# Kernel optimization log

Measured on AMD Instinct MI355X. Metric: run time of the kernel, lower is better.

Reference implementation:

```python
import jax, jax.numpy as jnp
import numpy as np

N_NODES = 50000
N_EDGES = 400000
NODE_DIM = 128
EDGE_DIM = 64
HIDDEN = 128  # must equal NODE_DIM (index_add into zeros_like(node_feat))
EPS = 1e-8


def _param(key, shape):
    fan_in = shape[0]
    return (jax.random.normal(key, shape, jnp.float32) / np.sqrt(fan_in)).astype(jnp.float32)


def setup_inputs() -> dict:
    key = jax.random.key(0)
    ks = jax.random.split(key, 20)
    inp = {
        'node_feat': jax.random.normal(ks[0], (N_NODES, NODE_DIM), jnp.float32),
        'edge_attr': jax.random.normal(ks[1], (N_EDGES, EDGE_DIM), jnp.float32),
        'coords': 5.0 * jax.random.normal(ks[2], (N_NODES, 3), jnp.float32),
        'edge_index': jax.random.randint(ks[3], (2, N_EDGES), 0, N_NODES, dtype=jnp.int32),
        # edge_mlp: Linear(2*node+edge -> hidden), SiLU, Linear(hidden -> hidden), SiLU
        'We1': _param(ks[4], (2 * NODE_DIM + EDGE_DIM, HIDDEN)),
        'be1': jnp.zeros((HIDDEN,), jnp.float32),
        'We2': _param(ks[5], (HIDDEN, HIDDEN)),
        'be2': jnp.zeros((HIDDEN,), jnp.float32),
        # node_mlp: Linear(node+hidden -> hidden), SiLU, Linear(hidden -> node)
        'Wn1': _param(ks[6], (NODE_DIM + HIDDEN, HIDDEN)),
        'bn1': jnp.zeros((HIDDEN,), jnp.float32),
        'Wn2': _param(ks[7], (HIDDEN, NODE_DIM)),
        'bn2': jnp.zeros((NODE_DIM,), jnp.float32),
        # coord_mlp: Linear(hidden -> hidden//2), SiLU, Linear(hidden//2 -> 1)
        'Wc1': _param(ks[8], (HIDDEN, HIDDEN // 2)),
        'bc1': jnp.zeros((HIDDEN // 2,), jnp.float32),
        'Wc2': _param(ks[9], (HIDDEN // 2, 1)),
        'bc2': jnp.zeros((1,), jnp.float32),
    }
    return inp


def reference(node_feat, edge_attr, coords, edge_index,
              We1, be1, We2, be2,
              Wn1, bn1, Wn2, bn2,
              Wc1, bc1, Wc2, bc2):
    src, dst = edge_index[0], edge_index[1]
    n_nodes = node_feat.shape[0]

    # gather -> edge MLP
    edge_feat = jnp.concatenate([node_feat[src], node_feat[dst], edge_attr], axis=-1)  # [E, 2*ND+ED]
    edge_message = jax.nn.silu(jax.nn.silu(edge_feat @ We1 + be1) @ We2 + be2)         # [E, H]

    # scatter-add messages to destination nodes
    aggr = jax.ops.segment_sum(edge_message, dst, num_segments=n_nodes)                # [N, H]

    # node update (residual)
    node_in = jnp.concatenate([node_feat, aggr], axis=-1)
    node_update = jax.nn.silu(node_in @ Wn1 + bn1) @ Wn2 + bn2
    updated_nodes = node_feat + node_update

    # equivariant coordinate update
    coord_w = jax.nn.silu(edge_message @ Wc1 + bc1) @ Wc2 + bc2                        # [E, 1]
    coord_diff = coords[src] - coords[dst]                                             # [E, 3]
    coord_diff = coord_diff / (jnp.linalg.norm(coord_diff, axis=-1, keepdims=True) + EPS)
    coord_update = jax.ops.segment_sum(coord_w * coord_diff, dst, num_segments=n_nodes)
    updated_coords = coords + coord_update

    return (updated_nodes, updated_coords)
```

## Files before the change

### kernel.cpp

```cpp
#include <hip/hip_runtime.h>
#include <hip/hip_bf16.h>
#include <math.h>
#include <stdint.h>

#define NN 50000
#define NE 400000

typedef __attribute__((ext_vector_type(8))) short short8;
typedef __attribute__((ext_vector_type(4))) float f32x4;

#define OFF_W1S  0
#define OFF_W1D  16384
#define OFF_W1E  32768
#define OFF_WE2T 40960
#define OFF_WN1T 57344
#define OFF_WN2T 90112
#define OFF_WC1T 106496
#define W_TOTAL  114688

__device__ __forceinline__ float silu_f(float x) {
    return x * (1.0f / (1.0f + __expf(-x)));
}
__device__ __forceinline__ short f2bf(float f) {
    __hip_bfloat16 b = __float2bfloat16(f);
    return *reinterpret_cast<short*>(&b);
}
__device__ __forceinline__ float bf2f(short s) {
    uint32_t u = ((uint32_t)(uint16_t)s) << 16;
    float f; __builtin_memcpy(&f, &u, 4); return f;
}
__device__ __forceinline__ uint32_t pk2(float lo, float hi) {
    return (uint32_t)(uint16_t)f2bf(lo) | ((uint32_t)(uint16_t)f2bf(hi) << 16);
}
__device__ __forceinline__ short8 cvt8(float4 a, float4 b) {
    short8 r;
    r[0] = f2bf(a.x); r[1] = f2bf(a.y); r[2] = f2bf(a.z); r[3] = f2bf(a.w);
    r[4] = f2bf(b.x); r[5] = f2bf(b.y); r[6] = f2bf(b.z); r[7] = f2bf(b.w);
    return r;
}

__device__ __forceinline__ short8 exch8(uint32_t e0, uint32_t e1,
                                        uint32_t o0, uint32_t o1,
                                        int g, int le) {
    const int srcA = le + 16 * ((g & 1) * 2);
    const int srcB = srcA + 16;
    const uint32_t a0e = __shfl((int)e0, srcA), a0o = __shfl((int)o0, srcA);
    const uint32_t a1e = __shfl((int)e1, srcA), a1o = __shfl((int)o1, srcA);
    const uint32_t b0e = __shfl((int)e0, srcB), b0o = __shfl((int)o0, srcB);
    const uint32_t b1e = __shfl((int)e1, srcB), b1o = __shfl((int)o1, srcB);
    const bool hi = (g & 2) != 0;
    uint32_t v[4];
    v[0] = hi ? a0o : a0e;  v[1] = hi ? a1o : a1e;
    v[2] = hi ? b0o : b0e;  v[3] = hi ? b1o : b1e;
    short8 r; __builtin_memcpy(&r, v, 16); return r;
}

__global__ void zero_kernel(float4* __restrict__ p, int n4) {
    int i = blockIdx.x * blockDim.x + threadIdx.x;
    int st = gridDim.x * blockDim.x;
    for (; i < n4; i += st) p[i] = make_float4(0.f, 0.f, 0.f, 0.f);
}

__global__ __launch_bounds__(256) void prep_kernel(
    const float* __restrict__ We1, const float* __restrict__ We2,
    const float* __restrict__ Wn1, const float* __restrict__ Wn2,
    const float* __restrict__ Wc1, short* __restrict__ wb)
{
    const int i = blockIdx.x * 256 + threadIdx.x;
    if (i >= W_TOTAL) return;
    float v; int rel, n, k;
    if (i < OFF_W1D)       { rel = i;            n = rel >> 7; k = rel & 127; v = We1[k * 128 + n]; }
    else if (i < OFF_W1E)  { rel = i - OFF_W1D;  n = rel >> 7; k = rel & 127; v = We1[(k + 128) * 128 + n]; }
    else if (i < OFF_WE2T) { rel = i - OFF_W1E;  n = rel >> 6; k = rel & 63;  v = We1[(k + 256) * 128 + n]; }
    else if (i < OFF_WN1T) { rel = i - OFF_WE2T; n = rel >> 7; k = rel & 127; v = We2[k * 128 + n]; }
    else if (i < OFF_WN2T) { rel = i - OFF_WN1T; n = rel >> 8; k = rel & 255; v = Wn1[k * 128 + n]; }
    else if (i < OFF_WC1T) { rel = i - OFF_WN2T; n = rel >> 7; k = rel & 127; v = Wn2[k * 128 + n]; }
    else                   { rel = i - OFF_WC1T; n = rel >> 7; k = rel & 127; v = Wc1[k * 64 + n]; }
    wb[i] = f2bf(v);
}

__global__ __launch_bounds__(256, 4) void ynode_kernel(
    const float* __restrict__ nf, const short* __restrict__ wb,
    short* __restrict__ ysb, short* __restrict__ ydb)
{
    const int tid = threadIdx.x;
    const int wv = tid >> 6, lane = tid & 63, le = lane & 15, grp = lane >> 4;
    const int nb = blockIdx.x * 128, wbase = wv * 32;
    const int row0 = min(nb + wbase + le, NN - 1);
    const int row1 = min(nb + wbase + 16 + le, NN - 1);

    #pragma unroll 1
    for (int pass = 0; pass < 2; ++pass) {
        const short* wt = wb + (pass ? OFF_W1D : OFF_W1S);
        short* op = pass ? ydb : ysb;

        f32x4 acc[2][8];
        #pragma unroll
        for (int m = 0; m < 2; ++m)
            #pragma unroll
            for (int t = 0; t < 8; ++t) acc[m][t] = (f32x4){0.f, 0.f, 0.f, 0.f};

        #pragma unroll
        for (int kc = 0; kc < 4; ++kc) {
            const int gk = kc * 32 + grp * 8;
            const float* p0 = nf + (size_t)row0 * 128 + gk;
            const float* p1 = nf + (size_t)row1 * 128 + gk;
            const short8 a0 = cvt8(*(const float4*)p0, *(const float4*)(p0 + 4));
            const short8 a1 = cvt8(*(const float4*)p1, *(const float4*)(p1 + 4));
            short8 bfv[8];
            #pragma unroll
            for (int t = 0; t < 8; ++t)
                bfv[t] = *(const short8*)(wt + (size_t)(t * 16 + le) * 128 + gk);
            #pragma unroll
            for (int t = 0; t < 8; ++t) {
                acc[0][t] = __builtin_amdgcn_mfma_f32_16x16x32_bf16(a0, bfv[t], acc[0][t], 0, 0, 0);
                acc[1][t] = __builtin_amdgcn_mfma_f32_16x16x32_bf16(a1, bfv[t], acc[1][t], 0, 0, 0);
            }
        }
        #pragma unroll
        for (int t = 0; t < 8; ++t)
            #pragma unroll
            for (int m = 0; m < 2; ++m)
                #pragma unroll
                for (int r = 0; r < 4; ++r) {
                    const int row = nb + wbase + m * 16 + grp * 4 + r;
                    if (row < NN)
                        op[(size_t)row * 128 + t * 16 + le] = f2bf(acc[m][t][r]);
                }
    }
}

__global__ __launch_bounds__(256, 4) void edge_kernel(
    const short* __restrict__ ysb, const short* __restrict__ ydb,
    const float* __restrict__ ea, const float* __restrict__ coords,
    const int* __restrict__ ei, const short* __restrict__ wb,
    const float* __restrict__ be1, const float* __restrict__ be2,
    const float* __restrict__ bc1, const float* __restrict__ bc2,
    const float* __restrict__ Wc2f,
    float* __restrict__ aggr, float* __restrict__ coord_acc)
{
    __shared__ float Ht4[4][16 * 136];

    const int tid = threadIdx.x;
    const int wv = tid >> 6, lane = tid & 63, le = lane & 15, g = lane >> 4;
    const int e = (blockIdx.x * 4 + wv) * 16 + le;
    float* Ht = Ht4[wv];

    const int s0 = ei[e], d0 = ei[NE + e];

    short8 ys8[4], yd8[4];
    #pragma unroll
    for (int cc = 0; cc < 4; ++cc) {
        ys8[cc] = *(const short8*)(ysb + (size_t)s0 * 128 + cc * 32 + g * 8);
        yd8[cc] = *(const short8*)(ydb + (size_t)d0 * 128 + cc * 32 + g * 8);
    }

    short8 eaB[2];
    #pragma unroll
    for (int kc = 0; kc < 2; ++kc) {
        const float* pe = ea + (size_t)e * 64 + kc * 32 + g * 8;
        eaB[kc] = cvt8(*(const float4*)pe, *(const float4*)(pe + 4));
    }

    f32x4 acc[8];
    #pragma unroll
    for (int t = 0; t < 8; ++t) acc[t] = (f32x4){0.f, 0.f, 0.f, 0.f};

    const short* w1e = wb + OFF_W1E;
    #pragma unroll
    for (int kc = 0; kc < 2; ++kc) {
        const int gk = kc * 32 + g * 8;
        short8 wfv[8];
        #pragma unroll
        for (int t = 0; t < 8; ++t)
            wfv[t] = *(const short8*)(w1e + (size_t)(t * 16 + le) * 64 + gk);
        #pragma unroll
        for (int t = 0; t < 8; ++t)
            acc[t] = __builtin_amdgcn_mfma_f32_16x16x32_bf16(wfv[t], eaB[kc], acc[t], 0, 0, 0);
    }

    uint32_t hp[8][2];
    #pragma unroll
    for (int t = 0; t < 8; ++t) {
        hp[t][0] = pk2(acc[t][0], acc[t][1]);
        hp[t][1] = pk2(acc[t][2], acc[t][3]);
    }

    short8 h1f[4];
    #pragma unroll
    for (int cc = 0; cc < 4; ++cc) {
        const short8 ex = exch8(hp[cc*2][0], hp[cc*2][1], hp[cc*2+1][0], hp[cc*2+1][1], g, le);
        const float* bp = be1 + cc * 32 + g * 8;
        #pragma unroll
        for (int j = 0; j < 8; ++j)
            h1f[cc][j] = f2bf(silu_f(bf2f(ex[j]) + bf2f(ys8[cc][j]) + bf2f(yd8[cc][j]) + bp[j]));
    }

    f32x4 acc2[8];
    #pragma unroll
    for (int t = 0; t < 8; ++t) acc2[t] = (f32x4){0.f, 0.f, 0.f, 0.f};

    const short* w2 = wb + OFF_WE2T;
    #pragma unroll
    for (int cc = 0; cc < 4; ++cc) {
        const int gk = cc * 32 + g * 8;
        short8 wfv[8];
        #pragma unroll
        for (int t = 0; t < 8; ++t)
            wfv[t] = *(const short8*)(w2 + (size_t)(t * 16 + le) * 128 + gk);
        #pragma unroll
        for (int t = 0; t < 8; ++t)
            acc2[t] = __builtin_amdgcn_mfma_f32_16x16x32_bf16(wfv[t], h1f[cc], acc2[t], 0, 0, 0);
    }

    #pragma unroll
    for (int t = 0; t < 8; ++t) {
        #pragma unroll
        for (int r = 0; r < 4; ++r) {
            const int col = t * 16 + g * 4 + r;
            Ht[le * 136 + col] = silu_f(acc2[t][r] + be2[col]);
        }
    }

    #pragma unroll
    for (int r = 0; r < 4; ++r) {
        const int er = g * 4 + r;
        const int dr = __shfl(d0, er);
        const float* hrow = &Ht[er * 136];
        #pragma unroll
        for (int t = 0; t < 8; ++t) {
            const int t2 = (t + g) & 7;
            atomicAdd(&aggr[(size_t)dr * 128 + t2 * 16 + le], hrow[t2 * 16 + le]);
        }
    }

    short8 h2f[4];
    #pragma unroll
    for (int cc = 0; cc < 4; ++cc) {
        const float* hq = &Ht[le * 136 + cc * 32 + g * 8];
        h2f[cc] = cvt8(*(const float4*)hq, *(const float4*)(hq + 4));
    }

    f32x4 acc3[4];
    #pragma unroll
    for (int t = 0; t < 4; ++t) acc3[t] = (f32x4){0.f, 0.f, 0.f, 0.f};

    const short* wc = wb + OFF_WC1T;
    #pragma unroll
    for (int cc = 0; cc < 4; ++cc) {
        const int gk = cc * 32 + g * 8;
        short8 wfv[4];
        #pragma unroll
        for (int t = 0; t < 4; ++t)
            wfv[t] = *(const short8*)(wc + (size_t)(t * 16 + le) * 128 + gk);
        #pragma unroll
        for (int t = 0; t < 4; ++t)
            acc3[t] = __builtin_amdgcn_mfma_f32_16x16x32_bf16(wfv[t], h2f[cc], acc3[t], 0, 0, 0);
    }

    float part = 0.f;
    #pragma unroll
    for (int t = 0; t < 4; ++t)
        #pragma unroll
        for (int r = 0; r < 4; ++r) {
            const int col = t * 16 + g * 4 + r;
            part += silu_f(acc3[t][r] + bc1[col]) * Wc2f[col];
        }
    part += __shfl_xor(part, 16);
    part += __shfl_xor(part, 32);

    if (g == 0) {
        const float wq = part + bc2[0];
        const float dx = coords[3 * s0 + 0] - coords[3 * d0 + 0];
        const float dy = coords[3 * s0 + 1] - coords[3 * d0 + 1];
        const float dz = coords[3 * s0 + 2] - coords[3 * d0 + 2];
        const float inv = wq / (sqrtf(dx * dx + dy * dy + dz * dz) + 1e-8f);
        atomicAdd(&coord_acc[3 * d0 + 0], dx * inv);
        atomicAdd(&coord_acc[3 * d0 + 1], dy * inv);
        atomicAdd(&coord_acc[3 * d0 + 2], dz * inv);
    }
}

__global__ __launch_bounds__(256, 2) void node_kernel(
    const float* __restrict__ nf, const float* __restrict__ coords,
    const short* __restrict__ wb,
    const float* __restrict__ bn1, const float* __restrict__ bn2,
    const float* __restrict__ aggr, const float* __restrict__ coord_acc,
    float* __restrict__ out)
{
    __shared__ short Hs[128][136];

    const int tid = threadIdx.x;
    const int wv = tid >> 6, lane = tid & 63, le = lane & 15, grp = lane >> 4;
    const int nb = blockIdx.x * 128, wbase = wv * 32;
    const int row0 = min(nb + wbase + le, NN - 1);
    const int row1 = min(nb + wbase + 16 + le, NN - 1);

    f32x4 acc[2][8];
    #pragma unroll
    for (int m = 0; m < 2; ++m)
        #pragma unroll
        for (int t = 0; t < 8; ++t) acc[m][t] = (f32x4){0.f, 0.f, 0.f, 0.f};

    const short* w1 = wb + OFF_WN1T;
    #pragma unroll
    for (int kc = 0; kc < 8; ++kc) {
        const int gk = kc * 32 + grp * 8;
        const float* p0 = (kc < 4) ? nf + (size_t)row0 * 128 + gk : aggr + (size_t)row0 * 128 + gk - 128;
        const float* p1 = (kc < 4) ? nf + (size_t)row1 * 128 + gk : aggr + (size_t)row1 * 128 + gk - 128;
        const short8 a0 = cvt8(*(const float4*)p0, *(const float4*)(p0 + 4));
        const short8 a1 = cvt8(*(const float4*)p1, *(const float4*)(p1 + 4));
        short8 bfv[8];
        #pragma unroll
        for (int t = 0; t < 8; ++t)
            bfv[t] = *(const short8*)(w1 + (size_t)(t * 16 + le) * 256 + gk);
        #pragma unroll
        for (int t = 0; t < 8; ++t) {
            acc[0][t] = __builtin_amdgcn_mfma_f32_16x16x32_bf16(a0, bfv[t], acc[0][t], 0, 0, 0);
            acc[1][t] = __builtin_amdgcn_mfma_f32_16x16x32_bf16(a1, bfv[t], acc[1][t], 0, 0, 0);
        }
    }
    #pragma unroll
    for (int t = 0; t < 8; ++t) {
        const float b1 = bn1[t * 16 + le];
        #pragma unroll
        for (int m = 0; m < 2; ++m)
            #pragma unroll
            for (int r = 0; r < 4; ++r)
                Hs[wbase + m * 16 + grp * 4 + r][t * 16 + le] = f2bf(silu_f(acc[m][t][r] + b1));
    }

    f32x4 acc2[2][8];
    #pragma unroll
    for (int m = 0; m < 2; ++m)
        #pragma unroll
        for (int t = 0; t < 8; ++t) acc2[m][t] = (f32x4){0.f, 0.f, 0.f, 0.f};

    const short* w2 = wb + OFF_WN2T;
    #pragma unroll
    for (int kc = 0; kc < 4; ++kc) {
        const int gk = kc * 32 + grp * 8;
        const short8 a0 = *(const short8*)&Hs[wbase + le][gk];
        const short8 a1 = *(const short8*)&Hs[wbase + 16 + le][gk];
        short8 bfv[8];
        #pragma unroll
        for (int t = 0; t < 8; ++t)
            bfv[t] = *(const short8*)(w2 + (size_t)(t * 16 + le) * 128 + gk);
        #pragma unroll
        for (int t = 0; t < 8; ++t) {
            acc2[0][t] = __builtin_amdgcn_mfma_f32_16x16x32_bf16(a0, bfv[t], acc2[0][t], 0, 0, 0);
            acc2[1][t] = __builtin_amdgcn_mfma_f32_16x16x32_bf16(a1, bfv[t], acc2[1][t], 0, 0, 0);
        }
    }
    #pragma unroll
    for (int t = 0; t < 8; ++t) {
        const float b2 = bn2[t * 16 + le];
        #pragma unroll
        for (int m = 0; m < 2; ++m)
            #pragma unroll
            for (int r = 0; r < 4; ++r) {
                const int row = nb + wbase + m * 16 + grp * 4 + r;
                if (row < NN) {
                    const int c = t * 16 + le;
                    out[(size_t)row * 128 + c] = acc2[m][t][r] + b2 + nf[(size_t)row * 128 + c];
                }
            }
    }

    for (int i = tid; i < 384; i += 256) {
        const int n = nb + i / 3, j = i % 3;
        if (n < NN)
            out[(size_t)NN * 128 + 3 * n + j] = coords[3 * n + j] + coord_acc[3 * n + j];
    }
}

extern "C" void kernel_launch(void* const* d_in, const int* in_sizes, int n_in,
                              void* d_out, int out_size, void* d_ws, size_t ws_size,
                              hipStream_t stream)
{
    const float* node_feat  = (const float*)d_in[0];
    const float* edge_attr  = (const float*)d_in[1];
    const float* coords     = (const float*)d_in[2];
    const int*   edge_index = (const int*)d_in[3];
    const float* We1 = (const float*)d_in[4];
    const float* be1 = (const float*)d_in[5];
    const float* We2 = (const float*)d_in[6];
    const float* be2 = (const float*)d_in[7];
    const float* Wn1 = (const float*)d_in[8];
    const float* bn1 = (const float*)d_in[9];
    const float* Wn2 = (const float*)d_in[10];
    const float* bn2 = (const float*)d_in[11];
    const float* Wc1 = (const float*)d_in[12];
    const float* bc1 = (const float*)d_in[13];
    const float* Wc2 = (const float*)d_in[14];
    const float* bc2 = (const float*)d_in[15];
    float* out = (float*)d_out;

    const size_t sz_wb  = (size_t)W_TOTAL * 2;
    const size_t sz_agg = (size_t)NN * 128 * 4;
    const size_t sz_cac = (size_t)NN * 3 * 4;
    const size_t sz_y   = (size_t)NN * 128 * 2;

    char* p = (char*)d_ws;
    short* wbf       = (short*)p;  p += sz_wb;
    float* aggr      = (float*)p;  p += sz_agg;
    float* coord_acc = (float*)p;  p += sz_cac;
    short* ysb       = (short*)p;  p += sz_y;
    short* ydb       = (short*)p;
    (void)ws_size;

    const int n4 = (NN * 128 + NN * 3) / 4;
    const int eg = NE / 64;
    const int ng = (NN + 127) / 128;

    prep_kernel<<<(W_TOTAL + 255) / 256, 256, 0, stream>>>(We1, We2, Wn1, Wn2, Wc1, wbf);
    zero_kernel<<<2048, 256, 0, stream>>>((float4*)aggr, n4);
    ynode_kernel<<<ng, 256, 0, stream>>>(node_feat, wbf, ysb, ydb);

    edge_kernel<<<eg, 256, 0, stream>>>(
        ysb, ydb, edge_attr, coords, edge_index, wbf,
        be1, be2, bc1, bc2, Wc2, aggr, coord_acc);

    node_kernel<<<ng, 256, 0, stream>>>(
        node_feat, coords, wbf, bn1, bn2, aggr, coord_acc, out);
}
```

Before: 390.0 us.

## Make edge kernel persistent with double-buffered async LDS prefetch of gathered rows

Turns the edge kernel into a persistent grid of 512 blocks whose waves loop over 16-edge tiles with a stride. The next tile's ysb/ydb rows are prefetched into a per-wave LDS double buffer via global_load_lds, and its edge_attr and indices are prefetched into registers, with a manual vmcnt wait. The intent is to hide gather latency behind the MFMA work. It also stores the second hidden layer as bf16 in LDS and feeds the coord MLP through shuffles instead of an fp32 LDS round trip. The cost is lower occupancy (launch bounds 2), a hand-tuned waitcnt that could go wrong, and bf16 rounding of the aggregated messages.

```diff
diff --git a/kernel.cpp b/kernel.cpp
--- a/kernel.cpp
+++ b/kernel.cpp
@@ -5,6 +5,8 @@
 
 #define NN 50000
 #define NE 400000
+#define NT 25000
+#define NWAVES 2048
 
 typedef __attribute__((ext_vector_type(8))) short short8;
 typedef __attribute__((ext_vector_type(4))) float f32x4;
@@ -53,6 +55,12 @@
     v[0] = hi ? a0o : a0e;  v[1] = hi ? a1o : a1e;
     v[2] = hi ? b0o : b0e;  v[3] = hi ? b1o : b1e;
     short8 r; __builtin_memcpy(&r, v, 16); return r;
+}
+
+__device__ __forceinline__ void gload16(const short* g, short* l) {
+    __builtin_amdgcn_global_load_lds(
+        (const __attribute__((address_space(1))) void*)g,
+        (__attribute__((address_space(3))) void*)l, 16, 0, 0);
 }
 
 __global__ void zero_kernel(float4* __restrict__ p, int n4) {
@@ -130,7 +138,7 @@
     }
 }
 
-__global__ __launch_bounds__(256, 4) void edge_kernel(
+__global__ __launch_bounds__(256, 2) void edge_kernel(
     const short* __restrict__ ysb, const short* __restrict__ ydb,
     const float* __restrict__ ea, const float* __restrict__ coords,
     const int* __restrict__ ei, const short* __restrict__ wb,
@@ -139,145 +147,188 @@
     const float* __restrict__ Wc2f,
     float* __restrict__ aggr, float* __restrict__ coord_acc)
 {
-    __shared__ float Ht4[4][16 * 136];
+    __shared__ short smem[4][2][4096];
 
     const int tid = threadIdx.x;
     const int wv = tid >> 6, lane = tid & 63, le = lane & 15, g = lane >> 4;
-    const int e = (blockIdx.x * 4 + wv) * 16 + le;
-    float* Ht = Ht4[wv];
-
-    const int s0 = ei[e], d0 = ei[NE + e];
-
-    short8 ys8[4], yd8[4];
+    const int t0 = blockIdx.x * 4 + wv;
+    if (t0 >= NT) return;
+
+    const short* w1e = wb + OFF_W1E;
+    const short* w2  = wb + OFF_WE2T;
+    const short* wc  = wb + OFF_WC1T;
+
+    int sc, dc, sn, dn;
+    float4 ea_c[4], ea_n[4];
+    {
+        const int e0 = t0 * 16 + le;
+        sc = ei[e0]; dc = ei[NE + e0];
+        const float* pe = ea + (size_t)e0 * 64 + g * 8;
+        ea_c[0] = *(const float4*)pe;        ea_c[1] = *(const float4*)(pe + 4);
+        ea_c[2] = *(const float4*)(pe + 32); ea_c[3] = *(const float4*)(pe + 36);
+    }
     #pragma unroll
     for (int cc = 0; cc < 4; ++cc) {
-        ys8[cc] = *(const short8*)(ysb + (size_t)s0 * 128 + cc * 32 + g * 8);
-        yd8[cc] = *(const short8*)(ydb + (size_t)d0 * 128 + cc * 32 + g * 8);
-    }
-
-    short8 eaB[2];
-    #pragma unroll
-    for (int kc = 0; kc < 2; ++kc) {
-        const float* pe = ea + (size_t)e * 64 + kc * 32 + g * 8;
-        eaB[kc] = cvt8(*(const float4*)pe, *(const float4*)(pe + 4));
-    }
-
-    f32x4 acc[8];
-    #pragma unroll
-    for (int t = 0; t < 8; ++t) acc[t] = (f32x4){0.f, 0.f, 0.f, 0.f};
-
-    const short* w1e = wb + OFF_W1E;
-    #pragma unroll
-    for (int kc = 0; kc < 2; ++kc) {
-        const int gk = kc * 32 + g * 8;
-        short8 wfv[8];
-        #pragma unroll
-        for (int t = 0; t < 8; ++t)
-            wfv[t] = *(const short8*)(w1e + (size_t)(t * 16 + le) * 64 + gk);
-        #pragma unroll
-        for (int t = 0; t < 8; ++t)
-            acc[t] = __builtin_amdgcn_mfma_f32_16x16x32_bf16(wfv[t], eaB[kc], acc[t], 0, 0, 0);
-    }
-
-    uint32_t hp[8][2];
-    #pragma unroll
-    for (int t = 0; t < 8; ++t) {
-        hp[t][0] = pk2(acc[t][0], acc[t][1]);
-        hp[t][1] = pk2(acc[t][2], acc[t][3]);
-    }
-
-    short8 h1f[4];
-    #pragma unroll
-    for (int cc = 0; cc < 4; ++cc) {
-        const short8 ex = exch8(hp[cc*2][0], hp[cc*2][1], hp[cc*2+1][0], hp[cc*2+1][1], g, le);
-        const float* bp = be1 + cc * 32 + g * 8;
-        #pragma unroll
-        for (int j = 0; j < 8; ++j)
-            h1f[cc][j] = f2bf(silu_f(bf2f(ex[j]) + bf2f(ys8[cc][j]) + bf2f(yd8[cc][j]) + bp[j]));
-    }
-
-    f32x4 acc2[8];
-    #pragma unroll
-    for (int t = 0; t < 8; ++t) acc2[t] = (f32x4){0.f, 0.f, 0.f, 0.f};
-
-    const short* w2 = wb + OFF_WE2T;
-    #pragma unroll
-    for (int cc = 0; cc < 4; ++cc) {
-        const int gk = cc * 32 + g * 8;
-        short8 wfv[8];
-        #pragma unroll
-        for (int t = 0; t < 8; ++t)
-            wfv[t] = *(const short8*)(w2 + (size_t)(t * 16 + le) * 128 + gk);
-        #pragma unroll
-        for (int t = 0; t < 8; ++t)
-            acc2[t] = __builtin_amdgcn_mfma_f32_16x16x32_bf16(wfv[t], h1f[cc], acc2[t], 0, 0, 0);
-    }
-
-    #pragma unroll
-    for (int t = 0; t < 8; ++t) {
+        gload16(ysb + (size_t)sc * 128 + cc * 32 + g * 8, &smem[wv][0][cc * 512]);
+        gload16(ydb + (size_t)dc * 128 + cc * 32 + g * 8, &smem[wv][0][2048 + cc * 512]);
+    }
+    {
+        const int t1 = (t0 + NWAVES < NT) ? t0 + NWAVES : t0;
+        const int e1 = t1 * 16 + le;
+        sn = ei[e1]; dn = ei[NE + e1];
+    }
+
+    int b = 0;
+    #pragma unroll 1
+    for (int t = t0; t < NT; t += NWAVES, b ^= 1) {
+        short* bufc = smem[wv][b];
+        short* bufn = smem[wv][b ^ 1];
+        const int s0 = sc, d0 = dc;
+
+        #pragma unroll
+        for (int cc = 0; cc < 4; ++cc) {
+            gload16(ysb + (size_t)sn * 128 + cc * 32 + g * 8, bufn + cc * 512);
+            gload16(ydb + (size_t)dn * 128 + cc * 32 + g * 8, bufn + 2048 + cc * 512);
+        }
+        {
+            const int tn = (t + NWAVES < NT) ? t + NWAVES : t;
+            const float* pe = ea + (size_t)(tn * 16 + le) * 64 + g * 8;
+            ea_n[0] = *(const float4*)pe;        ea_n[1] = *(const float4*)(pe + 4);
+            ea_n[2] = *(const float4*)(pe + 32); ea_n[3] = *(const float4*)(pe + 36);
+        }
+        int sf, df;
+        {
+            const int t2 = (t + 2 * NWAVES < NT) ? t + 2 * NWAVES : t;
+            const int e2 = t2 * 16 + le;
+            sf = ei[e2]; df = ei[NE + e2];
+        }
+
+        __builtin_amdgcn_sched_barrier(0);
+        asm volatile("s_waitcnt vmcnt(14)" ::: "memory");
+        __builtin_amdgcn_sched_barrier(0);
+
+        f32x4 acc[8];
+        #pragma unroll
+        for (int q = 0; q < 8; ++q) acc[q] = (f32x4){0.f, 0.f, 0.f, 0.f};
+        #pragma unroll
+        for (int kc = 0; kc < 2; ++kc) {
+            const short8 eaB = cvt8(ea_c[kc * 2], ea_c[kc * 2 + 1]);
+            const int gk = kc * 32 + g * 8;
+            short8 wfv[8];
+            #pragma unroll
+            for (int q = 0; q < 8; ++q)
+                wfv[q] = *(const short8*)(w1e + (size_t)(q * 16 + le) * 64 + gk);
+            #pragma unroll
+            for (int q = 0; q < 8; ++q)
+                acc[q] = __builtin_amdgcn_mfma_f32_16x16x32_bf16(wfv[q], eaB, acc[q], 0, 0, 0);
+        }
+        uint32_t hp[8][2];
+        #pragma unroll
+        for (int q = 0; q < 8; ++q) {
+            hp[q][0] = pk2(acc[q][0], acc[q][1]);
+            hp[q][1] = pk2(acc[q][2], acc[q][3]);
+        }
+
+        short8 h1f[4];
+        #pragma unroll
+        for (int cc = 0; cc < 4; ++cc) {
+            const short8 ys = *(const short8*)&bufc[cc * 512 + lane * 8];
+            const short8 yd = *(const short8*)&bufc[2048 + cc * 512 + lane * 8];
+            const short8 ex = exch8(hp[cc*2][0], hp[cc*2][1], hp[cc*2+1][0], hp[cc*2+1][1], g, le);
+            const float* bp = be1 + cc * 32 + g * 8;
+            #pragma unroll
+            for (int j = 0; j < 8; ++j)
+                h1f[cc][j] = f2bf(silu_f(bf2f(ex[j]) + bf2f(ys[j]) + bf2f(yd[j]) + bp[j]));
+        }
+
+        f32x4 acc2[8];
+        #pragma unroll
+        for (int q = 0; q < 8; ++q) acc2[q] = (f32x4){0.f, 0.f, 0.f, 0.f};
+        #pragma unroll
+        for (int cc = 0; cc < 4; ++cc) {
+            const int gk = cc * 32 + g * 8;
+            short8 wfv[8];
+            #pragma unroll
+            for (int q = 0; q < 8; ++q)
+                wfv[q] = *(const short8*)(w2 + (size_t)(q * 16 + le) * 128 + gk);
+            #pragma unroll
+            for (int q = 0; q < 8; ++q)
+                acc2[q] = __builtin_amdgcn_mfma_f32_16x16x32_bf16(wfv[q], h1f[cc], acc2[q], 0, 0, 0);
+        }
+
+        uint32_t hq[8][2];
+        #pragma unroll
+        for (int t8 = 0; t8 < 8; ++t8) {
+            float hv[4];
+            #pragma unroll
+            for (int r = 0; r < 4; ++r) {
+                const int col = t8 * 16 + g * 4 + r;
+                hv[r] = silu_f(acc2[t8][r] + be2[col]);
+            }
+            hq[t8][0] = pk2(hv[0], hv[1]);
+            hq[t8][1] = pk2(hv[2], hv[3]);
+            #pragma unroll
+            for (int r = 0; r < 4; ++r)
+                bufc[le * 136 + t8 * 16 + g * 4 + r] = f2bf(hv[r]);
+        }
+
         #pragma unroll
         for (int r = 0; r < 4; ++r) {
-            const int col = t * 16 + g * 4 + r;
-            Ht[le * 136 + col] = silu_f(acc2[t][r] + be2[col]);
-        }
-    }
-
-    #pragma unroll
-    for (int r = 0; r < 4; ++r) {
-        const int er = g * 4 + r;
-        const int dr = __shfl(d0, er);
-        const float* hrow = &Ht[er * 136];
-        #pragma unroll
-        for (int t = 0; t < 8; ++t) {
-            const int t2 = (t + g) & 7;
-            atomicAdd(&aggr[(size_t)dr * 128 + t2 * 16 + le], hrow[t2 * 16 + le]);
-        }
-    }
-
-    short8 h2f[4];
-    #pragma unroll
-    for (int cc = 0; cc < 4; ++cc) {
-        const float* hq = &Ht[le * 136 + cc * 32 + g * 8];
-        h2f[cc] = cvt8(*(const float4*)hq, *(const float4*)(hq + 4));
-    }
-
-    f32x4 acc3[4];
-    #pragma unroll
-    for (int t = 0; t < 4; ++t) acc3[t] = (f32x4){0.f, 0.f, 0.f, 0.f};
-
-    const short* wc = wb + OFF_WC1T;
-    #pragma unroll
-    for (int cc = 0; cc < 4; ++cc) {
-        const int gk = cc * 32 + g * 8;
-        short8 wfv[4];
-        #pragma unroll
-        for (int t = 0; t < 4; ++t)
-            wfv[t] = *(const short8*)(wc + (size_t)(t * 16 + le) * 128 + gk);
-        #pragma unroll
-        for (int t = 0; t < 4; ++t)
-            acc3[t] = __builtin_amdgcn_mfma_f32_16x16x32_bf16(wfv[t], h2f[cc], acc3[t], 0, 0, 0);
-    }
-
-    float part = 0.f;
-    #pragma unroll
-    for (int t = 0; t < 4; ++t)
-        #pragma unroll
-        for (int r = 0; r < 4; ++r) {
-            const int col = t * 16 + g * 4 + r;
-            part += silu_f(acc3[t][r] + bc1[col]) * Wc2f[col];
-        }
-    part += __shfl_xor(part, 16);
-    part += __shfl_xor(part, 32);
-
-    if (g == 0) {
-        const float wq = part + bc2[0];
-        const float dx = coords[3 * s0 + 0] - coords[3 * d0 + 0];
-        const float dy = coords[3 * s0 + 1] - coords[3 * d0 + 1];
-        const float dz = coords[3 * s0 + 2] - coords[3 * d0 + 2];
-        const float inv = wq / (sqrtf(dx * dx + dy * dy + dz * dz) + 1e-8f);
-        atomicAdd(&coord_acc[3 * d0 + 0], dx * inv);
-        atomicAdd(&coord_acc[3 * d0 + 1], dy * inv);
-        atomicAdd(&coord_acc[3 * d0 + 2], dz * inv);
+            const int er = g * 4 + r;
+            const int dr = __shfl(d0, er);
+            #pragma unroll
+            for (int t8 = 0; t8 < 8; ++t8) {
+                const int t2 = (t8 + g) & 7;
+                atomicAdd(&aggr[(size_t)dr * 128 + t2 * 16 + le],
+                          bf2f(bufc[er * 136 + t2 * 16 + le]));
+            }
+        }
+
+        short8 h2f[4];
+        #pragma unroll
+        for (int cc = 0; cc < 4; ++cc)
+            h2f[cc] = exch8(hq[cc*2][0], hq[cc*2][1], hq[cc*2+1][0], hq[cc*2+1][1], g, le);
+
+        f32x4 acc3[4];
+        #pragma unroll
+        for (int q = 0; q < 4; ++q) acc3[q] = (f32x4){0.f, 0.f, 0.f, 0.f};
+        #pragma unroll
+        for (int cc = 0; cc < 4; ++cc) {
+            const int gk = cc * 32 + g * 8;
+            short8 wfv[4];
+            #pragma unroll
+            for (int q = 0; q < 4; ++q)
+                wfv[q] = *(const short8*)(wc + (size_t)(q * 16 + le) * 128 + gk);
+            #pragma unroll
+            for (int q = 0; q < 4; ++q)
+                acc3[q] = __builtin_amdgcn_mfma_f32_16x16x32_bf16(wfv[q], h2f[cc], acc3[q], 0, 0, 0);
+        }
+
+        float part = 0.f;
+        #pragma unroll
+        for (int q = 0; q < 4; ++q)
+            #pragma unroll
+            for (int r = 0; r < 4; ++r) {
+                const int col = q * 16 + g * 4 + r;
+                part += silu_f(acc3[q][r] + bc1[col]) * Wc2f[col];
+            }
+        part += __shfl_xor(part, 16);
+        part += __shfl_xor(part, 32);
+
+        if (g == 0) {
+            const float wq = part + bc2[0];
+            const float dx = coords[3 * s0 + 0] - coords[3 * d0 + 0];
+            const float dy = coords[3 * s0 + 1] - coords[3 * d0 + 1];
+            const float dz = coords[3 * s0 + 2] - coords[3 * d0 + 2];
+            const float inv = wq / (sqrtf(dx * dx + dy * dy + dz * dz) + 1e-8f);
+            atomicAdd(&coord_acc[3 * d0 + 0], dx * inv);
+            atomicAdd(&coord_acc[3 * d0 + 1], dy * inv);
+            atomicAdd(&coord_acc[3 * d0 + 2], dz * inv);
+        }
+
+        sc = sn; dc = dn; sn = sf; dn = df;
+        #pragma unroll
+        for (int i = 0; i < 4; ++i) ea_c[i] = ea_n[i];
     }
 }
 
@@ -410,14 +461,13 @@
     (void)ws_size;
 
     const int n4 = (NN * 128 + NN * 3) / 4;
-    const int eg = NE / 64;
     const int ng = (NN + 127) / 128;
 
     prep_kernel<<<(W_TOTAL + 255) / 256, 256, 0, stream>>>(We1, We2, Wn1, Wn2, Wc1, wbf);
     zero_kernel<<<2048, 256, 0, stream>>>((float4*)aggr, n4);
     ynode_kernel<<<ng, 256, 0, stream>>>(node_feat, wbf, ysb, ydb);
 
-    edge_kernel<<<eg, 256, 0, stream>>>(
+    edge_kernel<<<512, 256, 0, stream>>>(
         ysb, ydb, edge_attr, coords, edge_index, wbf,
         be1, be2, bc1, bc2, Wc2, aggr, coord_acc);
 
```

Result: slower. 444.4 us (+14.0%).

## Sort edges by destination via CSR and pre-reduce scatter atomics

Applied to the files above, without the earlier changes.

Builds a destination-sorted edge permutation with histogram, three-stage scan and fill kernels, and has the edge kernel process edges in that order. Runs of edges sharing a destination within a 16-edge tile are summed in registers before issuing atomics, for both the hidden-feature aggregation and the coordinate update. This targets the heavy global atomic traffic into aggr, at the cost of several extra small launches, an indirect edge index lookup, and less sequential edge_attr reads.

```diff
diff --git a/kernel.cpp b/kernel.cpp
--- a/kernel.cpp
+++ b/kernel.cpp
@@ -79,6 +79,60 @@
     wb[i] = f2bf(v);
 }
 
+__global__ __launch_bounds__(256) void hist_kernel(const int* __restrict__ ei, int* __restrict__ cnt) {
+    const int e = blockIdx.x * 256 + threadIdx.x;
+    if (e < NE) atomicAdd(&cnt[ei[NE + e]], 1);
+}
+
+__global__ __launch_bounds__(256) void scanA_kernel(const int* __restrict__ cnt,
+                                                    int* __restrict__ eoff, int* __restrict__ bsum) {
+    __shared__ int sm[256];
+    const int t = threadIdx.x, idx = blockIdx.x * 256 + t;
+    const int v = (idx < NN) ? cnt[idx] : 0;
+    sm[t] = v; __syncthreads();
+    #pragma unroll
+    for (int o = 1; o < 256; o <<= 1) {
+        const int x = (t >= o) ? sm[t - o] : 0;
+        __syncthreads();
+        sm[t] += x;
+        __syncthreads();
+    }
+    if (idx < NN) eoff[idx] = sm[t] - v;
+    if (t == 255) bsum[blockIdx.x] = sm[255];
+}
+
+__global__ __launch_bounds__(256) void scanB_kernel(const int* __restrict__ bsum,
+                                                    int* __restrict__ bexcl, int nb) {
+    __shared__ int sm[256];
+    const int t = threadIdx.x;
+    const int v = (t < nb) ? bsum[t] : 0;
+    sm[t] = v; __syncthreads();
+    #pragma unroll
+    for (int o = 1; o < 256; o <<= 1) {
+        const int x = (t >= o) ? sm[t - o] : 0;
+        __syncthreads();
+        sm[t] += x;
+        __syncthreads();
+    }
+    bexcl[t] = sm[t] - v;
+}
+
+__global__ __launch_bounds__(256) void scanC_kernel(const int* __restrict__ eoff,
+                                                    const int* __restrict__ bexcl,
+                                                    int* __restrict__ cursor) {
+    const int idx = blockIdx.x * 256 + threadIdx.x;
+    if (idx < NN) cursor[idx] = eoff[idx] + bexcl[blockIdx.x];
+}
+
+__global__ __launch_bounds__(256) void fill_kernel(const int* __restrict__ ei,
+                                                   int* __restrict__ cursor, int* __restrict__ csr) {
+    const int e = blockIdx.x * 256 + threadIdx.x;
+    if (e < NE) {
+        const int pos = atomicAdd(&cursor[ei[NE + e]], 1);
+        csr[pos] = e;
+    }
+}
+
 __global__ __launch_bounds__(256, 4) void ynode_kernel(
     const float* __restrict__ nf, const short* __restrict__ wb,
     short* __restrict__ ysb, short* __restrict__ ydb)
@@ -133,7 +187,8 @@
 __global__ __launch_bounds__(256, 4) void edge_kernel(
     const short* __restrict__ ysb, const short* __restrict__ ydb,
     const float* __restrict__ ea, const float* __restrict__ coords,
-    const int* __restrict__ ei, const short* __restrict__ wb,
+    const int* __restrict__ ei, const int* __restrict__ csr,
+    const short* __restrict__ wb,
     const float* __restrict__ be1, const float* __restrict__ be2,
     const float* __restrict__ bc1, const float* __restrict__ bc2,
     const float* __restrict__ Wc2f,
@@ -143,7 +198,7 @@
 
     const int tid = threadIdx.x;
     const int wv = tid >> 6, lane = tid & 63, le = lane & 15, g = lane >> 4;
-    const int e = (blockIdx.x * 4 + wv) * 16 + le;
+    const int e = csr[(blockIdx.x * 4 + wv) * 16 + le];
     float* Ht = Ht4[wv];
 
     const int s0 = ei[e], d0 = ei[NE + e];
@@ -222,16 +277,25 @@
         }
     }
 
-    #pragma unroll
-    for (int r = 0; r < 4; ++r) {
-        const int er = g * 4 + r;
-        const int dr = __shfl(d0, er);
-        const float* hrow = &Ht[er * 136];
-        #pragma unroll
-        for (int t = 0; t < 8; ++t) {
-            const int t2 = (t + g) & 7;
-            atomicAdd(&aggr[(size_t)dr * 128 + t2 * 16 + le], hrow[t2 * 16 + le]);
-        }
+    {
+        const int c0 = g * 16 + le;
+        const int c1 = c0 + 64;
+        float a0 = 0.f, a1 = 0.f;
+        int dprev = __shfl(d0, 0);
+        #pragma unroll 1
+        for (int row = 0; row < 16; ++row) {
+            const int dr = __shfl(d0, row);
+            if (dr != dprev) {
+                atomicAdd(&aggr[(size_t)dprev * 128 + c0], a0);
+                atomicAdd(&aggr[(size_t)dprev * 128 + c1], a1);
+                a0 = 0.f; a1 = 0.f;
+                dprev = dr;
+            }
+            a0 += Ht[row * 136 + c0];
+            a1 += Ht[row * 136 + c1];
+        }
+        atomicAdd(&aggr[(size_t)dprev * 128 + c0], a0);
+        atomicAdd(&aggr[(size_t)dprev * 128 + c1], a1);
     }
 
     short8 h2f[4];
@@ -269,15 +333,30 @@
     part += __shfl_xor(part, 16);
     part += __shfl_xor(part, 32);
 
-    if (g == 0) {
-        const float wq = part + bc2[0];
-        const float dx = coords[3 * s0 + 0] - coords[3 * d0 + 0];
-        const float dy = coords[3 * s0 + 1] - coords[3 * d0 + 1];
-        const float dz = coords[3 * s0 + 2] - coords[3 * d0 + 2];
-        const float inv = wq / (sqrtf(dx * dx + dy * dy + dz * dz) + 1e-8f);
-        atomicAdd(&coord_acc[3 * d0 + 0], dx * inv);
-        atomicAdd(&coord_acc[3 * d0 + 1], dy * inv);
-        atomicAdd(&coord_acc[3 * d0 + 2], dz * inv);
+    const float wq = part + bc2[0];
+    const float dx = coords[3 * s0 + 0] - coords[3 * d0 + 0];
+    const float dy = coords[3 * s0 + 1] - coords[3 * d0 + 1];
+    const float dz = coords[3 * s0 + 2] - coords[3 * d0 + 2];
+    const float inv = wq / (sqrtf(dx * dx + dy * dy + dz * dz) + 1e-8f);
+    float vx = dx * inv, vy = dy * inv, vz = dz * inv;
+
+    {
+        const int prevd = __shfl(d0, (le == 0) ? 0 : (le - 1));
+        const bool head = (le == 0) || (prevd != d0);
+        float sx = vx, sy = vy, sz = vz;
+        #pragma unroll 1
+        for (int j = 1; j < 16; ++j) {
+            const float tx = __shfl(vx, le + j);
+            const float ty = __shfl(vy, le + j);
+            const float tz = __shfl(vz, le + j);
+            const int dj = __shfl(d0, le + j);
+            if ((le + j < 16) && (dj == d0)) { sx += tx; sy += ty; sz += tz; }
+        }
+        if (g == 0 && head) {
+            atomicAdd(&coord_acc[3 * d0 + 0], sx);
+            atomicAdd(&coord_acc[3 * d0 + 1], sy);
+            atomicAdd(&coord_acc[3 * d0 + 2], sz);
+        }
     }
 }
 
@@ -399,26 +478,41 @@
     const size_t sz_wb  = (size_t)W_TOTAL * 2;
     const size_t sz_agg = (size_t)NN * 128 * 4;
     const size_t sz_cac = (size_t)NN * 3 * 4;
+    const size_t sz_cnt = (size_t)NN * 4;
     const size_t sz_y   = (size_t)NN * 128 * 2;
 
     char* p = (char*)d_ws;
     short* wbf       = (short*)p;  p += sz_wb;
     float* aggr      = (float*)p;  p += sz_agg;
     float* coord_acc = (float*)p;  p += sz_cac;
+    int*   cnt       = (int*)p;    p += sz_cnt;
     short* ysb       = (short*)p;  p += sz_y;
-    short* ydb       = (short*)p;
+    short* ydb       = (short*)p;  p += sz_y;
+    int*   eoff      = (int*)p;    p += (size_t)NN * 4;
+    int*   bsum      = (int*)p;    p += 1024;
+    int*   bexcl     = (int*)p;    p += 1024;
+    int*   cursor    = (int*)p;    p += (size_t)NN * 4;
+    int*   csr       = (int*)p;
     (void)ws_size;
 
-    const int n4 = (NN * 128 + NN * 3) / 4;
+    const int n4 = (NN * 128 + NN * 3 + NN) / 4;
     const int eg = NE / 64;
     const int ng = (NN + 127) / 128;
+    const int eg256 = (NE + 255) / 256;
+    const int sg = (NN + 255) / 256;
 
     prep_kernel<<<(W_TOTAL + 255) / 256, 256, 0, stream>>>(We1, We2, Wn1, Wn2, Wc1, wbf);
     zero_kernel<<<2048, 256, 0, stream>>>((float4*)aggr, n4);
     ynode_kernel<<<ng, 256, 0, stream>>>(node_feat, wbf, ysb, ydb);
 
+    hist_kernel<<<eg256, 256, 0, stream>>>(edge_index, cnt);
+    scanA_kernel<<<sg, 256, 0, stream>>>(cnt, eoff, bsum);
+    scanB_kernel<<<1, 256, 0, stream>>>(bsum, bexcl, sg);
+    scanC_kernel<<<sg, 256, 0, stream>>>(eoff, bexcl, cursor);
+    fill_kernel<<<eg256, 256, 0, stream>>>(edge_index, cursor, csr);
+
     edge_kernel<<<eg, 256, 0, stream>>>(
-        ysb, ydb, edge_attr, coords, edge_index, wbf,
+        ysb, ydb, edge_attr, coords, edge_index, csr, wbf,
         be1, be2, bc1, bc2, Wc2, aggr, coord_acc);
 
     node_kernel<<<ng, 256, 0, stream>>>(
```

Measured after the change: 379.0 us. 1.03x faster.
